# Kernel tuning notes

Measured on AMD Instinct MI355X. Metric: run time of the kernel, lower is better.

Reference implementation:

```python
import jax, jax.numpy as jnp
import numpy as np

N_NODES = 500_000
N_EDGES = 2_500_000
N_GRAPHS = 1024


def _linear_params(key, fan_in, fan_out):
    # mimic torch.nn.Linear default init: U(-1/sqrt(fan_in), 1/sqrt(fan_in))
    k1, k2 = jax.random.split(key)
    bound = 1.0 / np.sqrt(fan_in)
    W = jax.random.uniform(k1, (fan_in, fan_out), jnp.float32, -bound, bound)
    b = jax.random.uniform(k2, (fan_out,), jnp.float32, -bound, bound)
    return W, b


def setup_inputs() -> dict:
    key = jax.random.key(0)
    ks = jax.random.split(key, 8)
    x = jax.random.normal(ks[0], (N_NODES, 2), jnp.float32)
    edge_index = jax.random.randint(ks[1], (2, N_EDGES), 0, N_NODES, jnp.int32)
    batch = jnp.sort(jax.random.randint(ks[2], (N_NODES,), 0, N_GRAPHS, jnp.int32))
    W1, b1 = _linear_params(ks[3], 2, 16)
    W2, b2 = _linear_params(ks[4], 16, 32)
    Wf1, bf1 = _linear_params(ks[5], 32, 16)
    Wf2, bf2 = _linear_params(ks[6], 16, 1)
    return {"x": x, "edge_index": edge_index, "batch": batch,
            "W1": W1, "b1": b1, "W2": W2, "b2": b2,
            "Wf1": Wf1, "bf1": bf1, "Wf2": Wf2, "bf2": bf2}


def _gnn_conv(h, W, b, src, dst, n_nodes):
    # Linear then add-aggregate: out[dst] += h_lin[src]  (self-loops already in src/dst)
    h = h @ W + b                       # [N, out]
    msgs = h[src]                       # gather over edges: [E+N, out]
    return jax.ops.segment_sum(msgs, dst, num_segments=n_nodes)


def reference(x, edge_index, batch, W1, b1, W2, b2, Wf1, bf1, Wf2, bf2):
    n = x.shape[0]
    loop = jnp.arange(n, dtype=edge_index.dtype)
    src = jnp.concatenate([edge_index[0], loop])  # source nodes (x_j)
    dst = jnp.concatenate([edge_index[1], loop])  # target nodes (aggregation index)

    h = jax.nn.relu(_gnn_conv(x, W1, b1, src, dst, n))   # [N, 16]
    h = jax.nn.relu(_gnn_conv(h, W2, b2, src, dst, n))   # [N, 32]

    # global mean pool per graph
    sums = jax.ops.segment_sum(h, batch, num_segments=N_GRAPHS)           # [G, 32]
    cnts = jax.ops.segment_sum(jnp.ones((n, 1), h.dtype), batch, num_segments=N_GRAPHS)
    pooled = sums / jnp.maximum(cnts, 1.0)

    out = jax.nn.relu(pooled @ Wf1 + bf1)
    out = out @ Wf2 + bf2                                # [G, 1]
    return out
```

## Files before the change

kernel.cpp:

```cpp
#include <hip/hip_runtime.h>


#define TPB 256
#define TPB1 512
#define SBK_BITS 8
#define SBK 256
#define NSBX 2048
#define CAPX 288
#define CAPS 1536
#define EWCAP (8 * CAPX)
#define PE1 4096
#define EPT (PE1 / TPB1)

typedef unsigned int uint32;

__device__ __forceinline__ float reluf(float v) { return v > 0.f ? v : 0.f; }

__global__ void kPart1(const int* __restrict__ src, const int* __restrict__ dst,
                       int* __restrict__ curx, int* __restrict__ part1x, int E) {
    __shared__ int h[NSBX];
    for (int i = threadIdx.x; i < NSBX; i += TPB1) h[i] = 0;
    __syncthreads();
    int base = blockIdx.x * PE1;
    int end = base + PE1 < E ? base + PE1 : E;
    int et = base + threadIdx.x;
    int rd[EPT];
#pragma unroll
    for (int k = 0; k < EPT; k++) {
        int e = et + k * TPB1;
        if (e < end) {
            int d = dst[e];
            rd[k] = d;
            atomicAdd(&h[d >> SBK_BITS], 1);
        }
    }
    __syncthreads();
    int slice = blockIdx.x & 7;
    int* cur = curx + slice * NSBX;
    int rbase = slice * (NSBX * CAPX);
    for (int i = threadIdx.x; i < NSBX; i += TPB1) {
        int c = h[i];
        if (c) h[i] = i * CAPX + atomicAdd(&cur[i], c);
    }
    __syncthreads();
#pragma unroll
    for (int k = 0; k < EPT; k++) {
        int e = et + k * TPB1;
        if (e < end) {
            int d = rd[k];
            int b = d >> SBK_BITS;
            int pos = atomicAdd(&h[b], 1);
            if (pos < (b + 1) * CAPX)
                part1x[rbase + pos] = (src[e] << SBK_BITS) | (d & (SBK - 1));
        }
    }
}

__global__ void kPart2C1(const int* __restrict__ curx, const int* __restrict__ part1x,
                         const float* __restrict__ x,
                         int* __restrict__ rowptr,
                         int* __restrict__ partS, uint2* __restrict__ ninfo,
                         float* __restrict__ pooled, float* __restrict__ cnts,
                         int N, int G) {
    int z = blockIdx.x * TPB + threadIdx.x;
    if (z < 32 * G) pooled[z] = 0.f;
    if (z < G) cnts[z] = 0.f;

    __shared__ int ew[EWCAP];
    __shared__ int sls[CAPS];
    __shared__ int hist[SBK];
    __shared__ int sstart[SBK];
    __shared__ int segc[8], soff[8];
    __shared__ int stot;
    __shared__ int wsum[4];
    int sb = blockIdx.x;
    int node0 = sb << SBK_BITS;
    int sbase = sb * CAPS;
    int t = threadIdx.x;
    hist[t] = 0;
    if (t < 8) {
        int c = curx[t * NSBX + sb];
        segc[t] = c > CAPX ? CAPX : c;
    }
    __syncthreads();
    if (t == 0) {
        int acc = 0;
        for (int s = 0; s < 8; s++) { soff[s] = acc; acc += segc[s]; }
        stot = acc;
    }
    __syncthreads();
    for (int seg = 0; seg < 8; seg++) {
        const int* p = part1x + seg * (NSBX * CAPX) + sb * CAPX;
        int c = segc[seg], o = soff[seg];
        for (int i = t; i < c; i += TPB) {
            int w = p[i];
            ew[o + i] = w;
            atomicAdd(&hist[w & (SBK - 1)], 1);
        }
    }
    __syncthreads();
    int tot = stot;
    int cnt = hist[t];
    int incl = cnt;
#pragma unroll
    for (int off = 1; off < 64; off <<= 1) {
        int u = __shfl_up(incl, off, 64);
        if ((t & 63) >= off) incl += u;
    }
    if ((t & 63) == 63) wsum[t >> 6] = incl;
    __syncthreads();
    int wid = t >> 6;
    int wpre = 0;
#pragma unroll
    for (int w = 0; w < 4; w++) wpre += (w < wid) ? wsum[w] : 0;
    int start = incl - cnt + wpre;
    sstart[t] = start;
    hist[t] = start;
    int n = node0 + t;
    if (n < N) rowptr[n] = sbase + start;
    __syncthreads();
    for (int i = t; i < tot; i += TPB) {
        int w = ew[i];
        int slot = atomicAdd(&hist[w & (SBK - 1)], 1);
        if (slot < CAPS) {
            int sid = w >> SBK_BITS;
            partS[sbase + slot] = sid;
            sls[slot] = sid;
        }
    }
    __syncthreads();
    if (n < N) {
        int st = sstart[t];
        int en0 = (t < SBK - 1) ? sstart[t + 1] : tot;
        int dg = en0 - st;
        int en = en0 > CAPS ? CAPS : en0;
        float2 sv = ((const float2*)x)[n];
        float a0 = sv.x, a1 = sv.y;
        for (int e = st; e < en; e++) {
            float2 xv = ((const float2*)x)[sls[e]];
            a0 += xv.x; a1 += xv.y;
        }
        int indeg = dg + 1;
        if (indeg > 31) indeg = 31;
        ninfo[n] = make_uint2(__float_as_uint(a0),
                              (__float_as_uint(a1) & ~31u) | (uint32)indeg);
    }
}

__device__ __forceinline__ void addMsg(float* a, uint2 q,
                                       const float* __restrict__ W1,
                                       const float* __restrict__ b1) {
    float n0 = __uint_as_float(q.x);
    float ndeg = (float)(q.y & 31u);
    float n1 = __uint_as_float(q.y & ~31u);
#pragma unroll
    for (int j = 0; j < 16; j++)
        a[j] += reluf(fmaf(n0, W1[j], fmaf(n1, W1[16 + j], ndeg * b1[j])));
}

__global__ void __launch_bounds__(TPB, 4)
kConv2(const uint2* __restrict__ ninfo, const int* __restrict__ partS,
       const int* __restrict__ rowptr, const int* __restrict__ batch,
       const float* __restrict__ W1, const float* __restrict__ b1,
       const float* __restrict__ W2, const float* __restrict__ b2,
       float* __restrict__ pooled, float* __restrict__ cnts, int N) {
    __shared__ float srow[TPB * 17];
    __shared__ int sbat[TPB];
    __shared__ float spart[16 * 16];
    __shared__ int scnt[16];
    int node0 = blockIdx.x * TPB;
    int l = threadIdx.x;
    int i = node0 + l;
    bool valid = i < N;
    float a[16];
    float sdeg = 0.f;
    if (valid) {
        uint2 p = ninfo[i];
        float s0 = __uint_as_float(p.x);
        sdeg = (float)(p.y & 31u);
        float s1 = __uint_as_float(p.y & ~31u);
        int rs = rowptr[i];
        int re = rs + (int)(p.y & 31u) - 1;
#pragma unroll
        for (int j = 0; j < 16; j++)
            a[j] = reluf(fmaf(s0, W1[j], fmaf(s1, W1[16 + j], sdeg * b1[j])));
        int e = rs;
        for (; e + 4 <= re; e += 4) {
            int w0 = partS[e], w1 = partS[e + 1], w2 = partS[e + 2], w3 = partS[e + 3];
            uint2 q0 = ninfo[w0], q1 = ninfo[w1], q2 = ninfo[w2], q3 = ninfo[w3];
            addMsg(a, q0, W1, b1);
            addMsg(a, q1, W1, b1);
            addMsg(a, q2, W1, b1);
            addMsg(a, q3, W1, b1);
        }
        for (; e < re; e++)
            addMsg(a, ninfo[partS[e]], W1, b1);
        sbat[l] = batch[i];
    } else {
#pragma unroll
        for (int j = 0; j < 16; j++) a[j] = 0.f;
        sbat[l] = -1;
    }
    __syncthreads();
    int nlast = node0 + TPB - 1;
    if (nlast > N - 1) nlast = N - 1;
    int g0 = batch[node0], g1 = batch[nlast];
    int f = l & 15, rr = l >> 4;
#pragma unroll
    for (int h = 0; h < 2; h++) {
        if (valid) {
#pragma unroll
            for (int jj = 0; jj < 16; jj++) {
                int j = h * 16 + jj;
                float vv = sdeg * b2[j];
#pragma unroll
                for (int k = 0; k < 16; k++) vv = fmaf(a[k], W2[k * 32 + j], vv);
                srow[l * 17 + jj] = reluf(vv);
            }
        } else {
#pragma unroll
            for (int jj = 0; jj < 16; jj++) srow[l * 17 + jj] = 0.f;
        }
        __syncthreads();
        for (int g = g0; g <= g1; g++) {
            float p = 0.f;
            int c = 0;
#pragma unroll
            for (int q = 0; q < 16; q++) {
                int n = rr + 16 * q;
                bool m = (sbat[n] == g);
                p += m ? srow[n * 17 + f] : 0.f;
                c += m ? 1 : 0;
            }
            spart[rr * 16 + f] = p;
            if (h == 0 && f == 0) scnt[rr] = c;
            __syncthreads();
            if (rr == 0) {
                float tot = 0.f;
#pragma unroll
                for (int q = 0; q < 16; q++) tot += spart[q * 16 + f];
                unsafeAtomicAdd(&pooled[32 * (size_t)g + h * 16 + f], tot);
            }
            if (h == 0 && l == 0) {
                int tc = 0;
#pragma unroll
                for (int q = 0; q < 16; q++) tc += scnt[q];
                if (tc) unsafeAtomicAdd(&cnts[g], (float)tc);
            }
            __syncthreads();
        }
        __syncthreads();
    }
}

__global__ void kMLP(const float* __restrict__ pooled, const float* __restrict__ cnts,
                     const float* __restrict__ Wf1, const float* __restrict__ bf1,
                     const float* __restrict__ Wf2, const float* __restrict__ bf2,
                     float* __restrict__ out, int G) {
    int g = blockIdx.x * blockDim.x + threadIdx.x;
    if (g >= G) return;
    float cf = cnts[g];
    float inv = 1.f / (cf > 1.f ? cf : 1.f);
    float p[32];
#pragma unroll
    for (int i = 0; i < 32; i++) p[i] = pooled[32 * (size_t)g + i] * inv;
    float acc = bf2[0];
#pragma unroll
    for (int j = 0; j < 16; j++) {
        float v = bf1[j];
#pragma unroll
        for (int i = 0; i < 32; i++) v = fmaf(p[i], Wf1[i * 16 + j], v);
        acc = fmaf(reluf(v), Wf2[j], acc);
    }
    out[g] = acc;
}

static inline size_t align256(size_t v) { return (v + 255) & ~(size_t)255; }

extern "C" void kernel_launch(void* const* d_in, const int* in_sizes, int n_in,
                              void* d_out, int out_size, void* d_ws, size_t ws_size,
                              hipStream_t stream) {
    const float* x    = (const float*)d_in[0];
    const int*   ei   = (const int*)d_in[1];
    const int*   batch= (const int*)d_in[2];
    const float* W1   = (const float*)d_in[3];
    const float* b1   = (const float*)d_in[4];
    const float* W2   = (const float*)d_in[5];
    const float* b2   = (const float*)d_in[6];
    const float* Wf1  = (const float*)d_in[7];
    const float* bf1  = (const float*)d_in[8];
    const float* Wf2  = (const float*)d_in[9];
    const float* bf2  = (const float*)d_in[10];
    float* out = (float*)d_out;

    const int N = in_sizes[0] / 2;
    const int E = in_sizes[1] / 2;
    const int G = out_size;
    const int* src = ei;
    const int* dst = ei + E;

    const int NSB = (N + SBK - 1) >> SBK_BITS;

    char* w = (char*)d_ws;
    int*   curx   = (int*)w;    w += align256((size_t)8 * NSBX * sizeof(int));
    int*   rowptr = (int*)w;    w += align256((size_t)N * sizeof(int));
    uint2* ninfo  = (uint2*)w;  w += align256((size_t)N * sizeof(uint2));
    float* pooled = (float*)w;  w += align256((size_t)G * 32 * sizeof(float));
    float* cnts   = (float*)w;  w += align256((size_t)G * sizeof(float));
    int*   part1x = (int*)w;    w += align256((size_t)8 * NSBX * CAPX * sizeof(int));
    int*   partS  = (int*)w;    w += align256((size_t)NSBX * CAPS * sizeof(int));

    const int nb1 = (E + PE1 - 1) / PE1;

    hipMemsetAsync(curx, 0, (size_t)8 * NSBX * sizeof(int), stream);
    kPart1  <<<nb1, TPB1, 0, stream>>>(src, dst, curx, part1x, E);
    kPart2C1<<<NSB, TPB, 0, stream>>>(curx, part1x, x, rowptr, partS,
                                      ninfo, pooled, cnts, N, G);
    kConv2  <<<NSB, TPB, 0, stream>>>(ninfo, partS, rowptr, batch,
                                      W1, b1, W2, b2, pooled, cnts, N);
    kMLP    <<<(G + TPB - 1) / TPB, TPB, 0, stream>>>(pooled, cnts, Wf1, bf1, Wf2, bf2, out, G);
}
```

Before: 178.3 us.

## Vectorize partition loads, drop rowptr array, fuse MLP into last conv block

kPart1 and kPart2C1 now read edge indices and partition data with int4 vector loads, and partS is written from shared memory in int4 chunks. The rowptr array is removed: kConv2 rebuilds per-node row starts with a block-local prefix scan over degrees packed in ninfo. The final MLP kernel is folded into kConv2 through a last-block-done atomic counter, which saves one launch. The int4 loads assume 16-byte aligned src/dst, i.e. E divisible by 4, and the serial tail MLP runs on a single block.

```diff
diff --git a/kernel.cpp b/kernel.cpp
--- a/kernel.cpp
+++ b/kernel.cpp
@@ -10,7 +10,6 @@
 #define CAPS 1536
 #define EWCAP (8 * CAPX)
 #define PE1 4096
-#define EPT (PE1 / TPB1)
 
 typedef unsigned int uint32;
 
@@ -23,42 +22,61 @@
     __syncthreads();
     int base = blockIdx.x * PE1;
     int end = base + PE1 < E ? base + PE1 : E;
-    int et = base + threadIdx.x;
-    int rd[EPT];
-#pragma unroll
-    for (int k = 0; k < EPT; k++) {
-        int e = et + k * TPB1;
-        if (e < end) {
-            int d = dst[e];
-            rd[k] = d;
-            atomicAdd(&h[d >> SBK_BITS], 1);
-        }
-    }
+    int t = threadIdx.x;
+    int nfull = (end - base) >> 2;
+    const int4* dst4 = (const int4*)(dst + base);
+    const int4* src4 = (const int4*)(src + base);
+    int4 rd4[2], rs4[2];
+#pragma unroll
+    for (int gi = 0; gi < 2; gi++) {
+        int g = t + gi * TPB1;
+        if (g < nfull) {
+            int4 d = dst4[g];
+            rd4[gi] = d;
+            rs4[gi] = src4[g];
+            atomicAdd(&h[d.x >> SBK_BITS], 1);
+            atomicAdd(&h[d.y >> SBK_BITS], 1);
+            atomicAdd(&h[d.z >> SBK_BITS], 1);
+            atomicAdd(&h[d.w >> SBK_BITS], 1);
+        }
+    }
+    for (int e = base + (nfull << 2) + t; e < end; e += TPB1)
+        atomicAdd(&h[dst[e] >> SBK_BITS], 1);
     __syncthreads();
     int slice = blockIdx.x & 7;
     int* cur = curx + slice * NSBX;
     int rbase = slice * (NSBX * CAPX);
-    for (int i = threadIdx.x; i < NSBX; i += TPB1) {
+    for (int i = t; i < NSBX; i += TPB1) {
         int c = h[i];
         if (c) h[i] = i * CAPX + atomicAdd(&cur[i], c);
     }
     __syncthreads();
 #pragma unroll
-    for (int k = 0; k < EPT; k++) {
-        int e = et + k * TPB1;
-        if (e < end) {
-            int d = rd[k];
-            int b = d >> SBK_BITS;
-            int pos = atomicAdd(&h[b], 1);
-            if (pos < (b + 1) * CAPX)
-                part1x[rbase + pos] = (src[e] << SBK_BITS) | (d & (SBK - 1));
-        }
+    for (int gi = 0; gi < 2; gi++) {
+        int g = t + gi * TPB1;
+        if (g < nfull) {
+            int d[4] = { rd4[gi].x, rd4[gi].y, rd4[gi].z, rd4[gi].w };
+            int s[4] = { rs4[gi].x, rs4[gi].y, rs4[gi].z, rs4[gi].w };
+#pragma unroll
+            for (int k = 0; k < 4; k++) {
+                int b = d[k] >> SBK_BITS;
+                int pos = atomicAdd(&h[b], 1);
+                if (pos < (b + 1) * CAPX)
+                    part1x[rbase + pos] = (s[k] << SBK_BITS) | (d[k] & (SBK - 1));
+            }
+        }
+    }
+    for (int e = base + (nfull << 2) + t; e < end; e += TPB1) {
+        int d = dst[e];
+        int b = d >> SBK_BITS;
+        int pos = atomicAdd(&h[b], 1);
+        if (pos < (b + 1) * CAPX)
+            part1x[rbase + pos] = (src[e] << SBK_BITS) | (d & (SBK - 1));
     }
 }
 
 __global__ void kPart2C1(const int* __restrict__ curx, const int* __restrict__ part1x,
                          const float* __restrict__ x,
-                         int* __restrict__ rowptr,
                          int* __restrict__ partS, uint2* __restrict__ ninfo,
                          float* __restrict__ pooled, float* __restrict__ cnts,
                          int N, int G) {
@@ -92,7 +110,17 @@
     for (int seg = 0; seg < 8; seg++) {
         const int* p = part1x + seg * (NSBX * CAPX) + sb * CAPX;
         int c = segc[seg], o = soff[seg];
-        for (int i = t; i < c; i += TPB) {
+        int c4 = c >> 2;
+        for (int i4 = t; i4 < c4; i4 += TPB) {
+            int4 w4 = ((const int4*)p)[i4];
+            int o4 = o + 4 * i4;
+            ew[o4] = w4.x; ew[o4 + 1] = w4.y; ew[o4 + 2] = w4.z; ew[o4 + 3] = w4.w;
+            atomicAdd(&hist[w4.x & (SBK - 1)], 1);
+            atomicAdd(&hist[w4.y & (SBK - 1)], 1);
+            atomicAdd(&hist[w4.z & (SBK - 1)], 1);
+            atomicAdd(&hist[w4.w & (SBK - 1)], 1);
+        }
+        for (int i = (c & ~3) + t; i < c; i += TPB) {
             int w = p[i];
             ew[o + i] = w;
             atomicAdd(&hist[w & (SBK - 1)], 1);
@@ -116,19 +144,18 @@
     int start = incl - cnt + wpre;
     sstart[t] = start;
     hist[t] = start;
-    int n = node0 + t;
-    if (n < N) rowptr[n] = sbase + start;
     __syncthreads();
     for (int i = t; i < tot; i += TPB) {
         int w = ew[i];
         int slot = atomicAdd(&hist[w & (SBK - 1)], 1);
-        if (slot < CAPS) {
-            int sid = w >> SBK_BITS;
-            partS[sbase + slot] = sid;
-            sls[slot] = sid;
-        }
-    }
-    __syncthreads();
+        if (slot < CAPS) sls[slot] = w >> SBK_BITS;
+    }
+    __syncthreads();
+    int texp = tot > CAPS ? CAPS : tot;
+    int e4 = (texp + 3) >> 2;
+    int4* pS4 = (int4*)(partS + sbase);
+    for (int i4 = t; i4 < e4; i4 += TPB) pS4[i4] = ((const int4*)sls)[i4];
+    int n = node0 + t;
     if (n < N) {
         int st = sstart[t];
         int en0 = (t < SBK - 1) ? sstart[t + 1] : tot;
@@ -160,31 +187,50 @@
 
 __global__ void __launch_bounds__(TPB, 4)
 kConv2(const uint2* __restrict__ ninfo, const int* __restrict__ partS,
-       const int* __restrict__ rowptr, const int* __restrict__ batch,
+       const int* __restrict__ batch,
        const float* __restrict__ W1, const float* __restrict__ b1,
        const float* __restrict__ W2, const float* __restrict__ b2,
-       float* __restrict__ pooled, float* __restrict__ cnts, int N) {
+       const float* __restrict__ Wf1, const float* __restrict__ bf1,
+       const float* __restrict__ Wf2, const float* __restrict__ bf2,
+       float* __restrict__ pooled, float* __restrict__ cnts,
+       float* __restrict__ out, int* __restrict__ ctr, int N, int G) {
     __shared__ float srow[TPB * 17];
     __shared__ int sbat[TPB];
     __shared__ float spart[16 * 16];
     __shared__ int scnt[16];
+    __shared__ int wsumC[4];
+    __shared__ int isLast;
     int node0 = blockIdx.x * TPB;
+    int sbase = blockIdx.x * CAPS;
     int l = threadIdx.x;
     int i = node0 + l;
     bool valid = i < N;
+    uint2 p = valid ? ninfo[i] : make_uint2(0u, 0u);
+    int dg = valid ? (int)(p.y & 31u) - 1 : 0;
+    int incl = dg;
+#pragma unroll
+    for (int off = 1; off < 64; off <<= 1) {
+        int u = __shfl_up(incl, off, 64);
+        if ((l & 63) >= off) incl += u;
+    }
+    if ((l & 63) == 63) wsumC[l >> 6] = incl;
+    __syncthreads();
+    int wid = l >> 6;
+    int wpre = 0;
+#pragma unroll
+    for (int w = 0; w < 4; w++) wpre += (w < wid) ? wsumC[w] : 0;
+    int st = incl - dg + wpre;
+    int en = st + dg; if (en > CAPS) en = CAPS;
     float a[16];
     float sdeg = 0.f;
     if (valid) {
-        uint2 p = ninfo[i];
         float s0 = __uint_as_float(p.x);
         sdeg = (float)(p.y & 31u);
         float s1 = __uint_as_float(p.y & ~31u);
-        int rs = rowptr[i];
-        int re = rs + (int)(p.y & 31u) - 1;
 #pragma unroll
         for (int j = 0; j < 16; j++)
             a[j] = reluf(fmaf(s0, W1[j], fmaf(s1, W1[16 + j], sdeg * b1[j])));
-        int e = rs;
+        int e = sbase + st, re = sbase + en;
         for (; e + 4 <= re; e += 4) {
             int w0 = partS[e], w1 = partS[e + 1], w2 = partS[e + 2], w3 = partS[e + 3];
             uint2 q0 = ninfo[w0], q1 = ninfo[w1], q2 = ninfo[w2], q3 = ninfo[w3];
@@ -223,16 +269,16 @@
         }
         __syncthreads();
         for (int g = g0; g <= g1; g++) {
-            float p = 0.f;
+            float pp = 0.f;
             int c = 0;
 #pragma unroll
             for (int q = 0; q < 16; q++) {
                 int n = rr + 16 * q;
                 bool m = (sbat[n] == g);
-                p += m ? srow[n * 17 + f] : 0.f;
+                pp += m ? srow[n * 17 + f] : 0.f;
                 c += m ? 1 : 0;
             }
-            spart[rr * 16 + f] = p;
+            spart[rr * 16 + f] = pp;
             if (h == 0 && f == 0) scnt[rr] = c;
             __syncthreads();
             if (rr == 0) {
@@ -251,28 +297,31 @@
         }
         __syncthreads();
     }
-}
-
-__global__ void kMLP(const float* __restrict__ pooled, const float* __restrict__ cnts,
-                     const float* __restrict__ Wf1, const float* __restrict__ bf1,
-                     const float* __restrict__ Wf2, const float* __restrict__ bf2,
-                     float* __restrict__ out, int G) {
-    int g = blockIdx.x * blockDim.x + threadIdx.x;
-    if (g >= G) return;
-    float cf = cnts[g];
-    float inv = 1.f / (cf > 1.f ? cf : 1.f);
-    float p[32];
-#pragma unroll
-    for (int i = 0; i < 32; i++) p[i] = pooled[32 * (size_t)g + i] * inv;
-    float acc = bf2[0];
-#pragma unroll
-    for (int j = 0; j < 16; j++) {
-        float v = bf1[j];
-#pragma unroll
-        for (int i = 0; i < 32; i++) v = fmaf(p[i], Wf1[i * 16 + j], v);
-        acc = fmaf(reluf(v), Wf2[j], acc);
-    }
-    out[g] = acc;
+    if (l == 0) {
+        __threadfence();
+        int r = __hip_atomic_fetch_add(ctr, 1, __ATOMIC_ACQ_REL, __HIP_MEMORY_SCOPE_AGENT);
+        isLast = (r == (int)gridDim.x - 1) ? 1 : 0;
+    }
+    __syncthreads();
+    if (!isLast) return;
+    for (int g = l; g < G; g += TPB) {
+        float cf = __hip_atomic_load(&cnts[g], __ATOMIC_RELAXED, __HIP_MEMORY_SCOPE_AGENT);
+        float inv = 1.f / (cf > 1.f ? cf : 1.f);
+        float pg[32];
+#pragma unroll
+        for (int q = 0; q < 32; q++)
+            pg[q] = __hip_atomic_load(&pooled[32 * (size_t)g + q],
+                                      __ATOMIC_RELAXED, __HIP_MEMORY_SCOPE_AGENT) * inv;
+        float acc = bf2[0];
+#pragma unroll
+        for (int j = 0; j < 16; j++) {
+            float v = bf1[j];
+#pragma unroll
+            for (int q = 0; q < 32; q++) v = fmaf(pg[q], Wf1[q * 16 + j], v);
+            acc = fmaf(reluf(v), Wf2[j], acc);
+        }
+        out[g] = acc;
+    }
 }
 
 static inline size_t align256(size_t v) { return (v + 255) & ~(size_t)255; }
@@ -302,8 +351,8 @@
     const int NSB = (N + SBK - 1) >> SBK_BITS;
 
     char* w = (char*)d_ws;
-    int*   curx   = (int*)w;    w += align256((size_t)8 * NSBX * sizeof(int));
-    int*   rowptr = (int*)w;    w += align256((size_t)N * sizeof(int));
+    int*   curx   = (int*)w;    w += (size_t)8 * NSBX * sizeof(int);
+    int*   ctr    = (int*)w;    w += 256;
     uint2* ninfo  = (uint2*)w;  w += align256((size_t)N * sizeof(uint2));
     float* pooled = (float*)w;  w += align256((size_t)G * 32 * sizeof(float));
     float* cnts   = (float*)w;  w += align256((size_t)G * sizeof(float));
@@ -312,11 +361,11 @@
 
     const int nb1 = (E + PE1 - 1) / PE1;
 
-    hipMemsetAsync(curx, 0, (size_t)8 * NSBX * sizeof(int), stream);
+    hipMemsetAsync(curx, 0, (size_t)8 * NSBX * sizeof(int) + 256, stream);
     kPart1  <<<nb1, TPB1, 0, stream>>>(src, dst, curx, part1x, E);
-    kPart2C1<<<NSB, TPB, 0, stream>>>(curx, part1x, x, rowptr, partS,
+    kPart2C1<<<NSB, TPB, 0, stream>>>(curx, part1x, x, partS,
                                       ninfo, pooled, cnts, N, G);
-    kConv2  <<<NSB, TPB, 0, stream>>>(ninfo, partS, rowptr, batch,
-                                      W1, b1, W2, b2, pooled, cnts, N);
-    kMLP    <<<(G + TPB - 1) / TPB, TPB, 0, stream>>>(pooled, cnts, Wf1, bf1, Wf2, bf2, out, G);
-}
+    kConv2  <<<NSB, TPB, 0, stream>>>(ninfo, partS, batch,
+                                      W1, b1, W2, b2, Wf1, bf1, Wf2, bf2,
+                                      pooled, cnts, out, ctr, N, G);
+}
```

After: 265.7 us. +49.0%, slower.
